# Optimization experiments

Hardware: AMD Instinct MI355X
Metric: run time of the kernel (lower is better)

The kernel has to match this reference:

```python
import jax, jax.numpy as jnp
import numpy as np

NH = 12        # main attention heads (head_dim = 64)
SNH = 4        # scorer self-attention heads
ALPHA = 0.1    # static survival-score weight
EPS = 1e-8


def _linear(x, w, b):
    # torch nn.Linear: y = x @ W^T + b
    return x @ w.T + b


def _mha(x, in_w, in_b, out_w, out_b, n_heads, maskf):
    # torch nn.MultiheadAttention (batch_first, eval mode)
    B, S, D = x.shape
    hd = D // n_heads
    qkv = _linear(x, in_w, in_b)                      # [B,S,3D]
    q, k, v = jnp.split(qkv, 3, axis=-1)
    sp = lambda t: t.reshape(B, S, n_heads, hd).transpose(0, 2, 1, 3)
    q, k, v = sp(q), sp(k), sp(v)                     # [B,h,S,hd]
    scores = jnp.einsum('bhqd,bhkd->bhqk', q, k) / jnp.asarray(np.sqrt(hd), x.dtype)
    scores = jnp.where(maskf[:, None, None, :] > 0, scores, jnp.asarray(-1e9, x.dtype))
    aw = jax.nn.softmax(scores, axis=-1)
    o = jnp.einsum('bhqk,bhkd->bhqd', aw, v).transpose(0, 2, 1, 3).reshape(B, S, D)
    return _linear(o, out_w, out_b)


def _survival_scores(x, maskf, sp_w, sp_b, sa_in_w, sa_in_b, sa_out_w, sa_out_b,
                     nw1, nb1, nw2, nb2, mw1, mb1, mw2, mb2, dw1, db1, dw2, db2):
    h = _linear(x, sp_w, sp_b)                        # [B,S,256]
    h = _mha(h, sa_in_w, sa_in_b, sa_out_w, sa_out_b, SNH, maskf)
    n = jax.nn.softplus(_linear(jax.nn.relu(_linear(h, nw1, nb1)), nw2, nb2))[..., 0]
    mu = jax.nn.sigmoid(_linear(jax.nn.relu(_linear(h, mw1, mb1)), mw2, mb2))[..., 0]
    delta = jax.nn.relu(_linear(jax.nn.relu(_linear(h, dw1, db1)), dw2, db2))[..., 0]
    # S = log(N) + log(mu / mu_c) - delta, with mu_c = 1.0
    return jnp.log(n + EPS) + jnp.log(mu + EPS) - delta


def setup_inputs() -> dict:
    key = jax.random.key(0)
    ks = iter(jax.random.split(key, 40))
    W = lambda shape: jax.random.normal(next(ks), shape, jnp.float32) * 0.05
    Z = lambda shape: jnp.zeros(shape, jnp.float32)
    B, S, H, I = 2, 2048, 768, 256
    inp = {
        'x': jax.random.normal(next(ks), (B, S, H), jnp.float32),
        'mask': jnp.ones((B, S), jnp.int32),
        'qw': W((H, H)), 'qb': Z((H,)),
        'kw': W((H, H)), 'kb': Z((H,)),
        'vw': W((H, H)), 'vb': Z((H,)),
        'ow': W((H, H)), 'ob': Z((H,)),
        'sp_w': W((I, H)), 'sp_b': Z((I,)),
        'sa_in_w': W((3 * I, I)), 'sa_in_b': Z((3 * I,)),
        'sa_out_w': W((I, I)), 'sa_out_b': Z((I,)),
        'nw1': W((I // 2, I)), 'nb1': Z((I // 2,)), 'nw2': W((1, I // 2)), 'nb2': Z((1,)),
        'mw1': W((I // 2, I)), 'mb1': Z((I // 2,)), 'mw2': W((1, I // 2)), 'mb2': Z((1,)),
        'dw1': W((I // 2, I)), 'db1': Z((I // 2,)), 'dw2': W((1, I // 2)), 'db2': Z((1,)),
    }
    return inp


def reference(x, mask, qw, qb, kw, kb, vw, vb, ow, ob,
              sp_w, sp_b, sa_in_w, sa_in_b, sa_out_w, sa_out_b,
              nw1, nb1, nw2, nb2, mw1, mb1, mw2, mb2, dw1, db1, dw2, db2):
    B, S, H = x.shape
    hd = H // NH
    maskf = mask.astype(x.dtype)
    # Q/K/V projections -> [B,h,S,hd]
    sp = lambda t: t.reshape(B, S, NH, hd).transpose(0, 2, 1, 3)
    q = sp(_linear(x, qw, qb))
    k = sp(_linear(x, kw, kb))
    v = sp(_linear(x, vw, vb))
    scores = jnp.einsum('bhqd,bhkd->bhqk', q, k) / jnp.asarray(np.sqrt(hd), x.dtype)
    # survival-score bias (broadcast over heads and query positions)
    surv = _survival_scores(x, maskf, sp_w, sp_b, sa_in_w, sa_in_b, sa_out_w, sa_out_b,
                            nw1, nb1, nw2, nb2, mw1, mb1, mw2, mb2, dw1, db1, dw2, db2)
    scores = scores + ALPHA * surv[:, None, None, :]
    scores = scores + (1.0 - maskf)[:, None, None, :] * -1e9
    aw = jax.nn.softmax(scores, axis=-1)
    out = jnp.einsum('bhqk,bhkd->bhqd', aw, v).transpose(0, 2, 1, 3).reshape(B, S, H)
    return _linear(out, ow, ob)
```

## Files before the change

### kernel.cpp

```cpp
#include <hip/hip_runtime.h>
#include <math.h>

typedef __bf16 bf16;
typedef __bf16 bfrag __attribute__((ext_vector_type(8)));
typedef __bf16 bf4 __attribute__((ext_vector_type(4)));
typedef float f4 __attribute__((ext_vector_type(4)));
typedef float f16v __attribute__((ext_vector_type(16)));
typedef unsigned uint2v __attribute__((ext_vector_type(2)));

#define LOG2E 1.4426950408889634f

#define DEV static __device__ __forceinline__

DEV f4 MFMA(bfrag a, bfrag b, f4 c) {
  return __builtin_amdgcn_mfma_f32_16x16x32_bf16(a, b, c, 0, 0, 0);
}
DEV f16v MFMA32(bfrag a, bfrag b, f16v c) {
  return __builtin_amdgcn_mfma_f32_32x32x16_bf16(a, b, c, 0, 0, 0);
}
DEV float ex2(float x) { return __builtin_amdgcn_exp2f(x); }
DEV uint2v pl32(unsigned a, unsigned b) {
  return __builtin_amdgcn_permlane32_swap(a, b, false, false);
}
DEV void gload_lds16(const bf16* g, bf16* l) {
  __builtin_amdgcn_global_load_lds(
      (const __attribute__((address_space(1))) void*)g,
      (__attribute__((address_space(3))) void*)l, 16, 0, 0);
}

__global__ __launch_bounds__(256) void pack_all(
    const float* __restrict__ x, const float* __restrict__ qw, const float* __restrict__ kw,
    const float* __restrict__ vw, const float* __restrict__ ow, const float* __restrict__ sp_w,
    const float* __restrict__ sa_in_w, const float* __restrict__ sa_out_w,
    const float* __restrict__ nw1, const float* __restrict__ mw1, const float* __restrict__ dw1,
    const float* __restrict__ sp_b, const float* __restrict__ qb, const float* __restrict__ kb,
    const float* __restrict__ vb,
    const float* __restrict__ nb1, const float* __restrict__ mb1, const float* __restrict__ db1,
    const int* __restrict__ mask,
    bf16* __restrict__ xb, bf16* __restrict__ wfused, bf16* __restrict__ wob,
    bf16* __restrict__ sainb, bf16* __restrict__ saoutb,
    bf16* __restrict__ w1pack, float* __restrict__ bfused, float* __restrict__ b1pack,
    float* __restrict__ maskBias) {
  int bid = blockIdx.x;
  int tid = threadIdx.x;
  const float* src = nullptr;
  bf16* dst = nullptr;
  int rel = 0;
  if (bid < 3072)      { src = x;       dst = xb;                   rel = bid; }
  else if (bid < 3264) { src = sp_w;    dst = wfused;               rel = bid - 3072; }
  else if (bid < 3840) { src = qw;      dst = wfused + 196608;      rel = bid - 3264; }
  else if (bid < 4416) { src = kw;      dst = wfused + 786432;      rel = bid - 3840; }
  else if (bid < 4992) { src = vw;      dst = wfused + 1376256;     rel = bid - 4416; }
  else if (bid < 5568) { src = ow;      dst = wob;                  rel = bid - 4992; }
  else if (bid < 5760) { src = sa_in_w; dst = sainb;                rel = bid - 5568; }
  else if (bid < 5824) { src = sa_out_w;dst = saoutb;               rel = bid - 5760; }
  else if (bid < 5856) { src = nw1;     dst = w1pack;               rel = bid - 5824; }
  else if (bid < 5888) { src = mw1;     dst = w1pack + 32768;       rel = bid - 5856; }
  else if (bid < 5920) { src = dw1;     dst = w1pack + 2 * 32768;   rel = bid - 5888; }
  else if (bid == 5920) {
    for (int t = tid; t < 640; t += 256) {
      const float* s;
      int j;
      if (t < 64)       { s = sp_b; j = t; }
      else if (t < 256) { s = qb;   j = t - 64; }
      else if (t < 448) { s = kb;   j = t - 256; }
      else              { s = vb;   j = t - 448; }
      reinterpret_cast<float4*>(bfused)[t] = reinterpret_cast<const float4*>(s)[j];
    }
    return;
  } else if (bid == 5921) {
    if (tid < 96) {
      int which = tid / 32, j = tid % 32;
      const float* s = which == 0 ? nb1 : (which == 1 ? mb1 : db1);
      reinterpret_cast<float4*>(b1pack)[tid] = reinterpret_cast<const float4*>(s)[j];
    }
    return;
  } else {
    int idx = (bid - 5922) * 256 + tid;
    int4 m = reinterpret_cast<const int4*>(mask)[idx];
    float4 o;
    o.x = m.x > 0 ? 0.f : -1e9f * LOG2E;
    o.y = m.y > 0 ? 0.f : -1e9f * LOG2E;
    o.z = m.z > 0 ? 0.f : -1e9f * LOG2E;
    o.w = m.w > 0 ? 0.f : -1e9f * LOG2E;
    reinterpret_cast<float4*>(maskBias)[idx] = o;
    return;
  }
  int i = rel * 256 + tid;
  float4 v = reinterpret_cast<const float4*>(src)[i];
  bf4 o;
  o[0] = (bf16)v.x; o[1] = (bf16)v.y; o[2] = (bf16)v.z; o[3] = (bf16)v.w;
  reinterpret_cast<bf4*>(dst)[i] = o;
}

template<int OUTF32, int RELU>
__global__ __launch_bounds__(256) void gemm_nt(
    const bf16* __restrict__ A, int lda,
    const bf16* __restrict__ W, int ldw,
    const float* __restrict__ bias,
    void* __restrict__ C, int ldc,
    int N64, int K) {
  int lane = threadIdx.x & 63;
  int w = threadIdx.x >> 6;
  int lrow = lane & 15, lgrp = lane >> 4;
  int tn = blockIdx.x % N64, tm = blockIdx.x / N64;
  int m0 = tm * 64 + (w >> 1) * 32;
  int n0 = tn * 64 + (w & 1) * 32;
  const bf16* Ab = A + (size_t)m0 * lda + lgrp * 8;
  const bf16* Wb = W + (size_t)n0 * ldw + lgrp * 8;
  f4 acc[2][2] = {};
  for (int k0 = 0; k0 < K; k0 += 32) {
    bfrag a0 = *(const bfrag*)(Ab + (size_t)lrow * lda + k0);
    bfrag a1 = *(const bfrag*)(Ab + (size_t)(lrow + 16) * lda + k0);
    bfrag b0 = *(const bfrag*)(Wb + (size_t)lrow * ldw + k0);
    bfrag b1 = *(const bfrag*)(Wb + (size_t)(lrow + 16) * ldw + k0);
    acc[0][0] = MFMA(a0, b0, acc[0][0]);
    acc[0][1] = MFMA(a0, b1, acc[0][1]);
    acc[1][0] = MFMA(a1, b0, acc[1][0]);
    acc[1][1] = MFMA(a1, b1, acc[1][1]);
  }
#pragma unroll
  for (int mi = 0; mi < 2; mi++)
#pragma unroll
    for (int nj = 0; nj < 2; nj++) {
      int col = n0 + nj * 16 + lrow;
      float bv = bias[col];
      int rowb = m0 + mi * 16 + lgrp * 4;
#pragma unroll
      for (int i = 0; i < 4; i++) {
        float v = acc[mi][nj][i] + bv;
        if (RELU) v = fmaxf(v, 0.f);
        if (OUTF32)
          ((float*)C)[(size_t)(rowb + i) * ldc + col] = v;
        else
          ((bf16*)C)[(size_t)(rowb + i) * ldc + col] = (bf16)v;
      }
    }
}

template<int OUTF32>
__global__ __launch_bounds__(256, 2) void gemm_big(
    const bf16* __restrict__ A,
    const bf16* __restrict__ W,
    const float* __restrict__ bias,
    void* __restrict__ C, int ldc,
    int N128, int K) {
  __shared__ char smem[65536];
  int lane = threadIdx.x & 63;
  int w = threadIdx.x >> 6;
  int lrow = lane & 15, lgrp = lane >> 4;
  int tn = blockIdx.x % N128, tm = blockIdx.x / N128;
  int m0 = tm * 128, n0 = tn * 128;

  int srow = lane >> 3;
  int sslot = (lane & 7) ^ srow;

  auto stage = [&](int bufb, int k0) {
#pragma unroll
    for (int j = 0; j < 4; j++) {
      int rb = (w * 4 + j) * 8 + srow;
      gload_lds16(A + (size_t)(m0 + rb) * K + k0 + sslot * 8,
                  (bf16*)(smem + bufb + (w * 4 + j) * 1024));
      gload_lds16(W + (size_t)(n0 + rb) * K + k0 + sslot * 8,
                  (bf16*)(smem + bufb + 16384 + (w * 4 + j) * 1024));
    }
  };

  f4 acc[4][4] = {};
  int swz = (lrow & 7) << 4;
  int mbase = (w >> 1) * 64, nbase = (w & 1) * 64;

  stage(0, 0);
  __syncthreads();
  int buf = 0;
  int nt = K / 64;
  for (int t = 0; t < nt; t++) {
    int nbuf = buf ^ 32768;
    if (t + 1 < nt) stage(nbuf, (t + 1) * 64);
    const char* As = smem + buf;
    const char* Ws = smem + buf + 16384;
#pragma unroll
    for (int kb = 0; kb < 128; kb += 64) {
      bfrag a[4], b[4];
#pragma unroll
      for (int i = 0; i < 4; i++) {
        a[i] = *(const bfrag*)(As + (mbase + i * 16 + lrow) * 128 + ((kb + lgrp * 16) ^ swz));
        b[i] = *(const bfrag*)(Ws + (nbase + i * 16 + lrow) * 128 + ((kb + lgrp * 16) ^ swz));
      }
#pragma unroll
      for (int mi = 0; mi < 4; mi++)
#pragma unroll
        for (int nj = 0; nj < 4; nj++)
          acc[mi][nj] = MFMA(a[mi], b[nj], acc[mi][nj]);
    }
    __syncthreads();
    buf = nbuf;
  }

#pragma unroll
  for (int mi = 0; mi < 4; mi++)
#pragma unroll
    for (int nj = 0; nj < 4; nj++) {
      int col = n0 + nbase + nj * 16 + lrow;
      float bv = bias[col];
      int rowb = m0 + mbase + mi * 16 + lgrp * 4;
#pragma unroll
      for (int i = 0; i < 4; i++) {
        float v = acc[mi][nj][i] + bv;
        if (OUTF32)
          ((float*)C)[(size_t)(rowb + i) * ldc + col] = v;
        else
          ((bf16*)C)[(size_t)(rowb + i) * ldc + col] = (bf16)v;
      }
    }
}

__global__ __launch_bounds__(256) void vtrans(const bf16* __restrict__ V, int rs, int coff,
                                              bf16* __restrict__ Vt, int H, int S) {
  int nst = S / 64;
  int st = blockIdx.x % nst;
  int h = (blockIdx.x / nst) % H;
  int b = blockIdx.x / (nst * H);
  __shared__ bf16 tile[64][72];
  int t = threadIdx.x;
  int r = t >> 2, c = t & 3;
  const bf16* src = V + ((size_t)b * S + st * 64 + r) * rs + coff + h * 64 + c * 16;
  bfrag v0 = *(const bfrag*)(src);
  bfrag v1 = *(const bfrag*)(src + 8);
  *(bfrag*)&tile[r][c * 16] = v0;
  *(bfrag*)&tile[r][c * 16 + 8] = v1;
  __syncthreads();
  bf16* dst = Vt + (((size_t)b * H + h) * 64 + r) * S + st * 64 + c * 16;
  bfrag o0, o1;
#pragma unroll
  for (int j = 0; j < 8; j++) {
    o0[j] = tile[c * 16 + j][r];
    o1[j] = tile[c * 16 + 8 + j][r];
  }
  *(bfrag*)dst = o0;
  *(bfrag*)(dst + 8) = o1;
}

template<int SPLIT, int PARTIAL>
__global__ __launch_bounds__(256) void flash9_k(
    const bf16* __restrict__ Q, const bf16* __restrict__ Kp, int rs,
    const bf16* __restrict__ Vt, const float* __restrict__ bias,
    bf16* __restrict__ O, int ors,
    float* __restrict__ Opart, float* __restrict__ Lpart,
    int H, int S, float scale, int Bc) {
  int nqt = S / 128;
  int bid = blockIdx.x;
  int qt = bid % nqt;
  int hh = (bid / nqt) % H;
  int b = (bid / (nqt * H)) % Bc;
  int sp = bid / (nqt * H * Bc);
  int lane = threadIdx.x & 63, w = threadIdx.x >> 6;
  int l31 = lane & 31, hf = lane >> 5;
  int q0 = qt * 128 + w * 32;
  const int kchunk = S / SPLIT;
  int k_beg = sp * kchunk;
  int swzl = (l31 & 7) << 4;

  const bf16* Qb = Q + ((size_t)b * S + q0 + l31) * rs + hh * 64 + hf * 8;
  bfrag qf[4];
#pragma unroll
  for (int c = 0; c < 4; c++) qf[c] = *(const bfrag*)(Qb + 16 * c);

  const bf16* gK0 = Kp + ((size_t)b * S + k_beg) * rs + hh * 64;
  const bf16* gV0 = Vt + (((size_t)b * H + hh) * 64) * (size_t)S + k_beg;
  const float* biasb = bias + (size_t)b * S;

  __shared__ bf16 KT[2][4096];
  __shared__ bf16 VT[2][4096];

  f16v acc0, acc1;
#pragma unroll
  for (int r = 0; r < 16; r++) { acc0[r] = 0.f; acc1[r] = 0.f; }
  float lrun = 0.f;

  int srow = lane >> 3;
  int sel = ((lane & 7) ^ srow) * 8;
  int r0 = (w * 2) * 8 + srow;
  int r1 = (w * 2 + 1) * 8 + srow;

  auto stage = [&](int bb, int trel) {
    const bf16* gK = gK0 + (size_t)trel * 64 * rs;
    const bf16* gV = gV0 + trel * 64;
    gload_lds16(gK + (size_t)r0 * rs + sel, KT[bb] + (w * 2) * 512);
    gload_lds16(gK + (size_t)r1 * rs + sel, KT[bb] + (w * 2 + 1) * 512);
    gload_lds16(gV + (size_t)r0 * S + sel, VT[bb] + (w * 2) * 512);
    gload_lds16(gV + (size_t)r1 * S + sel, VT[bb] + (w * 2 + 1) * 512);
  };

  stage(0, 0);
  __syncthreads();

  const int nt = kchunk / 64;
  int buf = 0;
  for (int t = 0; t < nt; t++) {
    int kt = k_beg + t * 64;
    if (t + 1 < nt) stage(buf ^ 1, t + 1);

    const char* KTb = (const char*)KT[buf];
    const char* VTb = (const char*)VT[buf];

    f16v s_lo, s_hi;
#pragma unroll
    for (int r = 0; r < 16; r++) { s_lo[r] = 0.f; s_hi[r] = 0.f; }
    __builtin_amdgcn_s_setprio(1);
#pragma unroll
    for (int c = 0; c < 4; c++) {
      int colb = 32 * c + 16 * hf;
      bfrag klo = *(const bfrag*)(KTb + l31 * 128 + (colb ^ swzl));
      bfrag khi = *(const bfrag*)(KTb + (32 + l31) * 128 + (colb ^ swzl));
      s_lo = MFMA32(klo, qf[c], s_lo);
      s_hi = MFMA32(khi, qf[c], s_hi);
    }
    __builtin_amdgcn_s_setprio(0);

    f4 blo[4], bhi[4];
#pragma unroll
    for (int g = 0; g < 4; g++) {
      blo[g] = *(const f4*)(biasb + kt + g * 8 + hf * 4);
      bhi[g] = *(const f4*)(biasb + kt + 32 + g * 8 + hf * 4);
    }
#pragma unroll
    for (int r = 0; r < 16; r++) {
      s_lo[r] = ex2(s_lo[r] * scale + blo[r >> 2][r & 3]);
      s_hi[r] = ex2(s_hi[r] * scale + bhi[r >> 2][r & 3]);
    }
    float rsum = s_lo[0] + s_hi[0];
#pragma unroll
    for (int r = 1; r < 16; r++) rsum += s_lo[r] + s_hi[r];
    rsum += __shfl_xor(rsum, 32);
    lrun += rsum;

    bfrag pb[4];
#pragma unroll
    for (int cc = 0; cc < 4; cc++) {
      const f16v& sv = (cc < 2) ? s_lo : s_hi;
      int rb = (cc & 1) * 8;
      unsigned lo0, lo1, hi0, hi1;
      asm("v_cvt_pk_bf16_f32 %0, %1, %2" : "=v"(lo0) : "v"(sv[rb + 0]), "v"(sv[rb + 1]));
      asm("v_cvt_pk_bf16_f32 %0, %1, %2" : "=v"(lo1) : "v"(sv[rb + 2]), "v"(sv[rb + 3]));
      asm("v_cvt_pk_bf16_f32 %0, %1, %2" : "=v"(hi0) : "v"(sv[rb + 4]), "v"(sv[rb + 5]));
      asm("v_cvt_pk_bf16_f32 %0, %1, %2" : "=v"(hi1) : "v"(sv[rb + 6]), "v"(sv[rb + 7]));
      uint2v e0 = pl32(lo0, hi0);
      uint2v e1 = pl32(lo1, hi1);
      union { bfrag v; unsigned u[4]; } pu;
      pu.u[0] = e0[0]; pu.u[1] = e1[0]; pu.u[2] = e0[1]; pu.u[3] = e1[1];
      pb[cc] = pu.v;
    }

    __builtin_amdgcn_s_setprio(1);
#pragma unroll
    for (int c = 0; c < 4; c++) {
      int colb = 32 * c + 16 * hf;
      bfrag v0 = *(const bfrag*)(VTb + l31 * 128 + (colb ^ swzl));
      bfrag v1 = *(const bfrag*)(VTb + (32 + l31) * 128 + (colb ^ swzl));
      acc0 = MFMA32(v0, pb[c], acc0);
      acc1 = MFMA32(v1, pb[c], acc1);
    }
    __builtin_amdgcn_s_setprio(0);

    __syncthreads();
    buf ^= 1;
  }

  int q = q0 + l31;
  if (PARTIAL) {
    float* op = Opart + ((((size_t)sp * Bc + b) * H + hh) * S + q) * 64 + hf * 4;
#pragma unroll
    for (int g = 0; g < 4; g++) {
      f4 v0, v1;
#pragma unroll
      for (int i = 0; i < 4; i++) { v0[i] = acc0[4 * g + i]; v1[i] = acc1[4 * g + i]; }
      *(f4*)(op + g * 8) = v0;
      *(f4*)(op + 32 + g * 8) = v1;
    }
    if (hf == 0)
      Lpart[(((size_t)sp * Bc + b) * H + hh) * S + q] = lrun;
  } else {
    float inv = 1.f / lrun;
    bf16* Ob = O + ((size_t)b * S + q) * ors + hh * 64 + hf * 4;
#pragma unroll
    for (int g = 0; g < 4; g++) {
      bf4 o0, o1;
#pragma unroll
      for (int i = 0; i < 4; i++) {
        o0[i] = (bf16)(acc0[4 * g + i] * inv);
        o1[i] = (bf16)(acc1[4 * g + i] * inv);
      }
      *(bf4*)(Ob + g * 8) = o0;
      *(bf4*)(Ob + 32 + g * 8) = o1;
    }
  }
}

__global__ __launch_bounds__(256) void flash_comb(
    const float* __restrict__ Opart, const float* __restrict__ L,
    bf16* __restrict__ O, int ors, int Hh, int S, int Bc, int nsplit) {
  int idx = blockIdx.x * 256 + threadIdx.x;
  int d4 = idx & 15;
  int q = (idx >> 4) % S;
  int hh = ((idx >> 4) / S) % Hh;
  int b = (idx >> 4) / (S * Hh);
  size_t rowstride = (size_t)Bc * Hh * S;
  size_t rbase = ((size_t)b * Hh + hh) * S + q;
  float lsum = 0.f;
  f4 o = {0.f, 0.f, 0.f, 0.f};
  for (int sp = 0; sp < nsplit; sp++) {
    lsum += L[sp * rowstride + rbase];
    f4 a = *(const f4*)(Opart + (sp * rowstride + rbase) * 64 + d4 * 4);
#pragma unroll
    for (int i = 0; i < 4; i++) o[i] += a[i];
  }
  float inv = 1.f / lsum;
  bf4 obv;
#pragma unroll
  for (int i = 0; i < 4; i++) obv[i] = (bf16)(o[i] * inv);
  *(bf4*)(O + ((size_t)b * S + q) * ors + hh * 64 + d4 * 4) = obv;
}

__global__ __launch_bounds__(256) void surv_k(
    const bf16* __restrict__ hid,
    const float* __restrict__ nw2, const float* __restrict__ nb2,
    const float* __restrict__ mw2, const float* __restrict__ mb2,
    const float* __restrict__ dw2, const float* __restrict__ db2,
    const float* __restrict__ maskBias, float* __restrict__ biasMain) {
  int w = threadIdx.x >> 6, lane = threadIdx.x & 63;
  int row = blockIdx.x * 4 + w;
  const bf16* hr = hid + (size_t)row * 384;
  const float* W2[3] = {nw2, mw2, dw2};
  float outs[3];
#pragma unroll
  for (int t = 0; t < 3; t++) {
    float acc = (float)hr[t * 128 + lane] * W2[t][lane] +
                (float)hr[t * 128 + 64 + lane] * W2[t][64 + lane];
    for (int msk = 1; msk < 64; msk <<= 1) acc += __shfl_xor(acc, msk);
    outs[t] = acc;
  }
  if (lane == 0) {
    float xn = outs[0] + nb2[0];
    float n = (xn > 20.f) ? xn : log1pf(__expf(xn));
    float mu = 1.f / (1.f + __expf(-(outs[1] + mb2[0])));
    float delta = fmaxf(outs[2] + db2[0], 0.f);
    float surv = logf(n + 1e-8f) + logf(mu + 1e-8f) - delta;
    biasMain[row] = 0.1f * LOG2E * surv + maskBias[row];
  }
}

extern "C" void kernel_launch(void* const* d_in, const int* in_sizes, int n_in,
                              void* d_out, int out_size, void* d_ws, size_t ws_size,
                              hipStream_t stream) {
  const int B = 2, S = 2048, H = 768, I = 256;
  const int NH = 12, SNH = 4;
  const int M = B * S;
  const int NF = 2560;
  const float SC = 0.125f * LOG2E;

  const float* x = (const float*)d_in[0];
  const int* mask = (const int*)d_in[1];
  const float* qw = (const float*)d_in[2];
  const float* qb = (const float*)d_in[3];
  const float* kw = (const float*)d_in[4];
  const float* kb = (const float*)d_in[5];
  const float* vw = (const float*)d_in[6];
  const float* vb = (const float*)d_in[7];
  const float* ow = (const float*)d_in[8];
  const float* ob = (const float*)d_in[9];
  const float* sp_w = (const float*)d_in[10];
  const float* sp_b = (const float*)d_in[11];
  const float* sa_in_w = (const float*)d_in[12];
  const float* sa_in_b = (const float*)d_in[13];
  const float* sa_out_w = (const float*)d_in[14];
  const float* sa_out_b = (const float*)d_in[15];
  const float* nw1 = (const float*)d_in[16];
  const float* nb1 = (const float*)d_in[17];
  const float* nw2 = (const float*)d_in[18];
  const float* nb2 = (const float*)d_in[19];
  const float* mw1 = (const float*)d_in[20];
  const float* mb1 = (const float*)d_in[21];
  const float* mw2 = (const float*)d_in[22];
  const float* mb2 = (const float*)d_in[23];
  const float* dw1 = (const float*)d_in[24];
  const float* db1 = (const float*)d_in[25];
  const float* dw2 = (const float*)d_in[26];
  const float* db2 = (const float*)d_in[27];

  char* ws = (char*)d_ws;
  size_t off = 0;
  auto alloc = [&](size_t bytes) -> void* {
    void* p = ws + off;
    off += (bytes + 255) & ~(size_t)255;
    return p;
  };

  bf16* xb = (bf16*)alloc((size_t)M * H * 2);
  bf16* wfused = (bf16*)alloc((size_t)NF * H * 2);
  float* bfused = (float*)alloc((size_t)NF * 4);
  bf16* wob = (bf16*)alloc((size_t)H * H * 2);
  bf16* sainb = (bf16*)alloc((size_t)(3 * I) * I * 2);
  bf16* saoutb = (bf16*)alloc((size_t)I * I * 2);
  bf16* w1pack = (bf16*)alloc((size_t)384 * 256 * 2);
  float* b1pack = (float*)alloc((size_t)384 * 4);
  float* maskBias = (float*)alloc((size_t)M * 4);
  float* biasMain = (float*)alloc((size_t)M * 4);
  bf16* Cfused = (bf16*)alloc((size_t)M * NF * 2);

  const int SPM = 2, SPS = 4;
  size_t offMark = off;
  bf16* qkv_s = (bf16*)alloc((size_t)M * (3 * I) * 2);
  bf16* vt_s = (bf16*)alloc((size_t)B * SNH * 64 * S * 2);
  bf16* attn_s = (bf16*)alloc((size_t)M * I * 2);
  bf16* h1 = (bf16*)alloc((size_t)M * I * 2);
  bf16* hid = (bf16*)alloc((size_t)M * 384 * 2);
  float* Opart_s = (float*)alloc((size_t)SPS * B * SNH * S * 64 * 4);
  float* L_s = (float*)alloc((size_t)SPS * B * SNH * S * 4);
  size_t endA = off;
  off = offMark;
  bf16* vt_m = (bf16*)alloc((size_t)B * NH * 64 * S * 2);
  bf16* attn_m = (bf16*)alloc((size_t)M * H * 2);
  float* Opart_m = (float*)alloc((size_t)SPM * B * NH * S * 64 * 4);
  float* L_m = (float*)alloc((size_t)SPM * B * NH * S * 4);
  size_t endB = off;
  size_t need = endA > endB ? endA : endB;
  bool split_ok = ws_size >= need;
  (void)in_sizes; (void)n_in; (void)out_size;

  pack_all<<<5926, 256, 0, stream>>>(x, qw, kw, vw, ow, sp_w, sa_in_w, sa_out_w, nw1, mw1, dw1,
                                     sp_b, qb, kb, vb, nb1, mb1, db1, mask,
                                     xb, wfused, wob, sainb, saoutb, w1pack, bfused, b1pack,
                                     maskBias);

  gemm_big<0><<<(M / 128) * (NF / 128), 256, 0, stream>>>(xb, wfused, bfused, Cfused, NF,
                                                          NF / 128, H);

  gemm_nt<0, 0><<<(M / 64) * ((3 * I) / 64), 256, 0, stream>>>(Cfused, NF, sainb, I, sa_in_b,
                                                               qkv_s, 3 * I, (3 * I) / 64, I);
  vtrans<<<B * SNH * (S / 64), 256, 0, stream>>>(qkv_s, 3 * I, 2 * I, vt_s, SNH, S);
  if (split_ok) {
    flash9_k<SPS, 1><<<SPS * B * SNH * (S / 128), 256, 0, stream>>>(
        qkv_s, qkv_s + I, 3 * I, vt_s, maskBias, nullptr, 0, Opart_s, L_s, SNH, S, SC, B);
    flash_comb<<<(B * SNH * S * 16) / 256, 256, 0, stream>>>(Opart_s, L_s, attn_s, I, SNH, S,
                                                             B, SPS);
  } else {
    flash9_k<1, 0><<<B * SNH * (S / 128), 256, 0, stream>>>(
        qkv_s, qkv_s + I, 3 * I, vt_s, maskBias, attn_s, I, nullptr, nullptr, SNH, S, SC, B);
  }
  gemm_nt<0, 0><<<(M / 64) * (I / 64), 256, 0, stream>>>(attn_s, I, saoutb, I, sa_out_b, h1, I,
                                                         I / 64, I);
  gemm_nt<0, 1><<<(M / 64) * (384 / 64), 256, 0, stream>>>(h1, I, w1pack, I, b1pack, hid, 384,
                                                           384 / 64, I);
  surv_k<<<M / 4, 256, 0, stream>>>(hid, nw2, nb2, mw2, mb2, dw2, db2, maskBias, biasMain);

  vtrans<<<B * NH * (S / 64), 256, 0, stream>>>(Cfused, NF, 1792, vt_m, NH, S);
  if (split_ok) {
    flash9_k<SPM, 1><<<SPM * B * NH * (S / 128), 256, 0, stream>>>(
        Cfused + 256, Cfused + 1024, NF, vt_m, biasMain, nullptr, 0, Opart_m, L_m, NH, S, SC,
        B);
    flash_comb<<<(B * NH * S * 16) / 256, 256, 0, stream>>>(Opart_m, L_m, attn_m, H, NH, S, B,
                                                            SPM);
  } else {
    flash9_k<1, 0><<<B * NH * (S / 128), 256, 0, stream>>>(
        Cfused + 256, Cfused + 1024, NF, vt_m, biasMain, attn_m, H, nullptr, nullptr, NH, S,
        SC, B);
  }
  gemm_big<1><<<(M / 128) * (H / 128), 256, 0, stream>>>(attn_m, wob, ob, d_out, H,
                                                         H / 128, H);
}
```

Measured before the change: 176.1 us.

## Store split-K attention partials in bf16, remap blocks per XCD, raise main split

Split-K flash partial outputs are now written and read as bf16 instead of fp32, halving partial-buffer traffic between the flash kernel and the combine kernel. Block indices are permuted so consecutive work lands across the 8 XCDs in a strided pattern, which may improve L2 locality for K/V sharing. The main attention split factor goes from 2 to 4 for more parallelism, and the bias loads are hoisted ahead of the QK MFMAs to hide latency. Rounding unnormalized partial sums to bf16 adds some precision loss, and the extra split adds combine work.

```diff
diff --git a/kernel.cpp b/kernel.cpp
--- a/kernel.cpp
+++ b/kernel.cpp
@@ -242,14 +242,16 @@
 }
 
 template<int SPLIT, int PARTIAL>
-__global__ __launch_bounds__(256) void flash9_k(
+__global__ __launch_bounds__(256) void flash10_k(
     const bf16* __restrict__ Q, const bf16* __restrict__ Kp, int rs,
     const bf16* __restrict__ Vt, const float* __restrict__ bias,
     bf16* __restrict__ O, int ors,
-    float* __restrict__ Opart, float* __restrict__ Lpart,
+    bf16* __restrict__ Opart, float* __restrict__ Lpart,
     int H, int S, float scale, int Bc) {
   int nqt = S / 128;
-  int bid = blockIdx.x;
+  int nwg8 = (gridDim.x >> 3);
+  int bid0 = blockIdx.x;
+  int bid = (bid0 & 7) * nwg8 + (bid0 >> 3);
   int qt = bid % nqt;
   int hh = (bid / nqt) % H;
   int b = (bid / (nqt * H)) % Bc;
@@ -268,7 +270,7 @@
 
   const bf16* gK0 = Kp + ((size_t)b * S + k_beg) * rs + hh * 64;
   const bf16* gV0 = Vt + (((size_t)b * H + hh) * 64) * (size_t)S + k_beg;
-  const float* biasb = bias + (size_t)b * S;
+  const float* biasb = bias + (size_t)b * S + k_beg;
 
   __shared__ bf16 KT[2][4096];
   __shared__ bf16 VT[2][4096];
@@ -298,8 +300,14 @@
   const int nt = kchunk / 64;
   int buf = 0;
   for (int t = 0; t < nt; t++) {
-    int kt = k_beg + t * 64;
     if (t + 1 < nt) stage(buf ^ 1, t + 1);
+
+    f4 blo[4], bhi[4];
+#pragma unroll
+    for (int g = 0; g < 4; g++) {
+      blo[g] = *(const f4*)(biasb + t * 64 + g * 8 + hf * 4);
+      bhi[g] = *(const f4*)(biasb + t * 64 + 32 + g * 8 + hf * 4);
+    }
 
     const char* KTb = (const char*)KT[buf];
     const char* VTb = (const char*)VT[buf];
@@ -318,12 +326,6 @@
     }
     __builtin_amdgcn_s_setprio(0);
 
-    f4 blo[4], bhi[4];
-#pragma unroll
-    for (int g = 0; g < 4; g++) {
-      blo[g] = *(const f4*)(biasb + kt + g * 8 + hf * 4);
-      bhi[g] = *(const f4*)(biasb + kt + 32 + g * 8 + hf * 4);
-    }
 #pragma unroll
     for (int r = 0; r < 16; r++) {
       s_lo[r] = ex2(s_lo[r] * scale + blo[r >> 2][r & 3]);
@@ -369,14 +371,17 @@
 
   int q = q0 + l31;
   if (PARTIAL) {
-    float* op = Opart + ((((size_t)sp * Bc + b) * H + hh) * S + q) * 64 + hf * 4;
+    bf16* op = Opart + ((((size_t)sp * Bc + b) * H + hh) * S + q) * 64 + hf * 4;
 #pragma unroll
     for (int g = 0; g < 4; g++) {
-      f4 v0, v1;
-#pragma unroll
-      for (int i = 0; i < 4; i++) { v0[i] = acc0[4 * g + i]; v1[i] = acc1[4 * g + i]; }
-      *(f4*)(op + g * 8) = v0;
-      *(f4*)(op + 32 + g * 8) = v1;
+      bf4 v0, v1;
+#pragma unroll
+      for (int i = 0; i < 4; i++) {
+        v0[i] = (bf16)acc0[4 * g + i];
+        v1[i] = (bf16)acc1[4 * g + i];
+      }
+      *(bf4*)(op + g * 8) = v0;
+      *(bf4*)(op + 32 + g * 8) = v1;
     }
     if (hf == 0)
       Lpart[(((size_t)sp * Bc + b) * H + hh) * S + q] = lrun;
@@ -398,7 +403,7 @@
 }
 
 __global__ __launch_bounds__(256) void flash_comb(
-    const float* __restrict__ Opart, const float* __restrict__ L,
+    const bf16* __restrict__ Opart, const float* __restrict__ L,
     bf16* __restrict__ O, int ors, int Hh, int S, int Bc, int nsplit) {
   int idx = blockIdx.x * 256 + threadIdx.x;
   int d4 = idx & 15;
@@ -411,9 +416,9 @@
   f4 o = {0.f, 0.f, 0.f, 0.f};
   for (int sp = 0; sp < nsplit; sp++) {
     lsum += L[sp * rowstride + rbase];
-    f4 a = *(const f4*)(Opart + (sp * rowstride + rbase) * 64 + d4 * 4);
-#pragma unroll
-    for (int i = 0; i < 4; i++) o[i] += a[i];
+    bf4 a = *(const bf4*)(Opart + (sp * rowstride + rbase) * 64 + d4 * 4);
+#pragma unroll
+    for (int i = 0; i < 4; i++) o[i] += (float)a[i];
   }
   float inv = 1.f / lsum;
   bf4 obv;
@@ -508,20 +513,20 @@
   float* biasMain = (float*)alloc((size_t)M * 4);
   bf16* Cfused = (bf16*)alloc((size_t)M * NF * 2);
 
-  const int SPM = 2, SPS = 4;
+  const int SPM = 4, SPS = 4;
   size_t offMark = off;
   bf16* qkv_s = (bf16*)alloc((size_t)M * (3 * I) * 2);
   bf16* vt_s = (bf16*)alloc((size_t)B * SNH * 64 * S * 2);
   bf16* attn_s = (bf16*)alloc((size_t)M * I * 2);
   bf16* h1 = (bf16*)alloc((size_t)M * I * 2);
   bf16* hid = (bf16*)alloc((size_t)M * 384 * 2);
-  float* Opart_s = (float*)alloc((size_t)SPS * B * SNH * S * 64 * 4);
+  bf16* Opart_s = (bf16*)alloc((size_t)SPS * B * SNH * S * 64 * 2);
   float* L_s = (float*)alloc((size_t)SPS * B * SNH * S * 4);
   size_t endA = off;
   off = offMark;
   bf16* vt_m = (bf16*)alloc((size_t)B * NH * 64 * S * 2);
   bf16* attn_m = (bf16*)alloc((size_t)M * H * 2);
-  float* Opart_m = (float*)alloc((size_t)SPM * B * NH * S * 64 * 4);
+  bf16* Opart_m = (bf16*)alloc((size_t)SPM * B * NH * S * 64 * 2);
   float* L_m = (float*)alloc((size_t)SPM * B * NH * S * 4);
   size_t endB = off;
   size_t need = endA > endB ? endA : endB;
@@ -540,12 +545,12 @@
                                                                qkv_s, 3 * I, (3 * I) / 64, I);
   vtrans<<<B * SNH * (S / 64), 256, 0, stream>>>(qkv_s, 3 * I, 2 * I, vt_s, SNH, S);
   if (split_ok) {
-    flash9_k<SPS, 1><<<SPS * B * SNH * (S / 128), 256, 0, stream>>>(
+    flash10_k<SPS, 1><<<SPS * B * SNH * (S / 128), 256, 0, stream>>>(
         qkv_s, qkv_s + I, 3 * I, vt_s, maskBias, nullptr, 0, Opart_s, L_s, SNH, S, SC, B);
     flash_comb<<<(B * SNH * S * 16) / 256, 256, 0, stream>>>(Opart_s, L_s, attn_s, I, SNH, S,
                                                              B, SPS);
   } else {
-    flash9_k<1, 0><<<B * SNH * (S / 128), 256, 0, stream>>>(
+    flash10_k<1, 0><<<B * SNH * (S / 128), 256, 0, stream>>>(
         qkv_s, qkv_s + I, 3 * I, vt_s, maskBias, attn_s, I, nullptr, nullptr, SNH, S, SC, B);
   }
   gemm_nt<0, 0><<<(M / 64) * (I / 64), 256, 0, stream>>>(attn_s, I, saoutb, I, sa_out_b, h1, I,
@@ -556,13 +561,13 @@
 
   vtrans<<<B * NH * (S / 64), 256, 0, stream>>>(Cfused, NF, 1792, vt_m, NH, S);
   if (split_ok) {
-    flash9_k<SPM, 1><<<SPM * B * NH * (S / 128), 256, 0, stream>>>(
+    flash10_k<SPM, 1><<<SPM * B * NH * (S / 128), 256, 0, stream>>>(
         Cfused + 256, Cfused + 1024, NF, vt_m, biasMain, nullptr, 0, Opart_m, L_m, NH, S, SC,
         B);
     flash_comb<<<(B * NH * S * 16) / 256, 256, 0, stream>>>(Opart_m, L_m, attn_m, H, NH, S, B,
                                                             SPM);
   } else {
-    flash9_k<1, 0><<<B * NH * (S / 128), 256, 0, stream>>>(
+    flash10_k<1, 0><<<B * NH * (S / 128), 256, 0, stream>>>(
         Cfused + 256, Cfused + 1024, NF, vt_m, biasMain, attn_m, H, nullptr, nullptr, NH, S,
         SC, B);
   }
```

Result: no change. 177.2 us (+0.6%).
